# Performance work log

Measured on AMD Instinct MI355X. Metric: run time of the kernel, lower is better.

## Reference

```python
import jax, jax.numpy as jnp
import numpy as np

B = 4; P = 4096; N = B * P          # octree leaf nodes at this depth, equal per sample
ND = N // 8; K = 27                 # stride-2 output nodes; 3x3x3 stencil taps
CIN = 128; COUT = 256; G = 32       # channels, groupnorm groups
H = 16; DH = COUT // H              # attention heads
LCTX = 77; CTX = 768                # context tokens / dim
EPS = 1e-5


def octree_conv(x, neigh, W, b):
    # x: [M_in, Cin], neigh: [M_out, K] (-1 = missing neighbor), W: [K, Cin, Cout]
    mask = (neigh >= 0).astype(x.dtype)[..., None]
    g = x[jnp.maximum(neigh, 0)] * mask            # [M_out, K, Cin]
    return jnp.einsum('nkc,kcd->nd', g, W) + b


def octree_group_norm(x, gamma, beta):
    # per-sample, per-group stats over (nodes-in-sample, channels-in-group)
    n, c = x.shape
    xr = x.reshape(B, n // B, G, c // G)
    mean = xr.mean(axis=(1, 3), keepdims=True)
    var = xr.var(axis=(1, 3), keepdims=True)
    xn = (xr - mean) * jax.lax.rsqrt(var + EPS)
    return xn.reshape(n, c) * gamma + beta


def layer_norm(x, w, b):
    mu = x.mean(-1, keepdims=True)
    var = x.var(-1, keepdims=True)
    return (x - mu) * jax.lax.rsqrt(var + EPS) * w + b


def cross_attention(x, context, ln_w, ln_b, wq, bq, wk, bk, wv, bv, wo, bo):
    # equal points per sample -> per-sample ragged loop == batched attention
    xn = layer_norm(x, ln_w, ln_b).reshape(B, P, COUT)
    q = (xn @ wq + bq).reshape(B, P, H, DH)
    k = (context @ wk + bk).reshape(B, LCTX, H, DH)
    v = (context @ wv + bv).reshape(B, LCTX, H, DH)
    scores = jnp.einsum('bphd,blhd->bhpl', q, k) / np.float32(np.sqrt(DH))
    attn = jax.nn.softmax(scores, axis=-1)
    o = jnp.einsum('bhpl,blhd->bphd', attn, v).reshape(B, P, COUT)
    return x + (o @ wo + bo).reshape(N, COUT)


def reference(x, context, neigh, neigh_down,
              g1_w, g1_b, conv1_w, conv1_b, g2_w, g2_b, conv2_w, conv2_b,
              sc_w, sc_b, ln_w, ln_b, wq, bq, wk, bk, wv, bv, wo, bo,
              down_w, down_b):
    # ResnetBlock
    res = x
    h = jax.nn.silu(octree_group_norm(x, g1_w, g1_b))
    h = octree_conv(h, neigh, conv1_w, conv1_b)
    h = jax.nn.silu(octree_group_norm(h, g2_w, g2_b))
    h = octree_conv(h, neigh, conv2_w, conv2_b)
    h = h + (res @ sc_w + sc_b)                      # Conv1x1 shortcut, skip_scale=1
    # CrossAttention
    h = cross_attention(h, context, ln_w, ln_b, wq, bq, wk, bk, wv, bv, wo, bo)
    # stride-2 downsample conv
    x_down = octree_conv(h, neigh_down, down_w, down_b)
    return (x_down, h)


def setup_inputs():
    key = jax.random.key(0)
    ks = jax.random.split(key, 16)
    w = lambda k, shape, s=0.02: jax.random.normal(k, shape, jnp.float32) * s
    return dict(
        x=w(ks[0], (N, CIN), 1.0),
        context=w(ks[1], (B, LCTX, CTX), 1.0),
        neigh=jax.random.randint(ks[2], (N, K), -3, N, dtype=jnp.int32),
        neigh_down=jax.random.randint(ks[3], (ND, K), -3, N, dtype=jnp.int32),
        g1_w=jnp.ones(CIN), g1_b=jnp.zeros(CIN),
        conv1_w=w(ks[4], (K, CIN, COUT)), conv1_b=jnp.zeros(COUT),
        g2_w=jnp.ones(COUT), g2_b=jnp.zeros(COUT),
        conv2_w=w(ks[5], (K, COUT, COUT)), conv2_b=jnp.zeros(COUT),
        sc_w=w(ks[6], (CIN, COUT)), sc_b=jnp.zeros(COUT),
        ln_w=jnp.ones(COUT), ln_b=jnp.zeros(COUT),
        wq=w(ks[7], (COUT, COUT)), bq=jnp.zeros(COUT),
        wk=w(ks[8], (CTX, COUT)), bk=jnp.zeros(COUT),
        wv=w(ks[9], (CTX, COUT)), bv=jnp.zeros(COUT),
        wo=w(ks[10], (COUT, COUT)), bo=jnp.zeros(COUT),
        down_w=w(ks[11], (K, COUT, COUT)), down_b=jnp.zeros(COUT),
    )
```

## Files before the change

kernel.cpp:

```cpp
#include <hip/hip_runtime.h>
#include <stdint.h>

typedef unsigned short u16;
typedef unsigned int   u32;
typedef __attribute__((ext_vector_type(8))) __bf16 bf16x8;
typedef __attribute__((ext_vector_type(4))) float  f32x4;

__device__ __forceinline__ float bflo(u32 u){ return __uint_as_float(u << 16); }
__device__ __forceinline__ float bfhi(u32 u){ return __uint_as_float(u & 0xffff0000u); }
__device__ __forceinline__ float bf2f(u16 v){ return __uint_as_float(((u32)v) << 16); }
__device__ __forceinline__ u16 f2bf(float f){ u32 u = __float_as_uint(f);
    return (u16)((u + 0x7fffu + ((u >> 16) & 1u)) >> 16); }
__device__ __forceinline__ u32 pack2(float a, float b){ return (u32)f2bf(a) | ((u32)f2bf(b) << 16); }

union ABu { f32x4 f; bf16x8 b; };
__device__ __forceinline__ bf16x8 ldfrag(const u16* p){ ABu u; u.f = *(const f32x4*)p; return u.b; }

__global__ void zero_kernel(u32* p){ p[threadIdx.x] = 0u; }

__global__ __launch_bounds__(256) void bias_init(float* out, const float* b)
{ out[(size_t)blockIdx.x * 256 + threadIdx.x] = b[threadIdx.x]; }

__global__ __launch_bounds__(256)
void transpose_one(const float* __restrict__ in, u16* __restrict__ out, int R)
{
    const int r0 = blockIdx.y * 32, c0 = blockIdx.x * 32;
    __shared__ u16 t[32][33];
    const int tx = threadIdx.x & 31, ty = threadIdx.x >> 5;
    #pragma unroll
    for (int i = 0; i < 4; ++i)
        t[ty + i*8][tx] = f2bf(in[(size_t)(r0 + ty + i*8) * 256 + c0 + tx]);
    __syncthreads();
    #pragma unroll
    for (int i = 0; i < 4; ++i)
        out[(size_t)(c0 + ty + i*8) * R + r0 + tx] = t[tx][ty + i*8];
}

template<int C, int CPG, int IF32>
__global__ __launch_bounds__(256)
void gn_silu_kernel(const void* __restrict__ xv, const float* __restrict__ gw,
                    const float* __restrict__ gb, u16* __restrict__ y)
{
    const int b = blockIdx.x >> 5, g = blockIdx.x & 31;
    const size_t base = (size_t)b * 4096 * C + g * CPG;
    float s = 0.f, ss = 0.f;
    for (int p = threadIdx.x; p < 4096; p += 256) {
        if constexpr (IF32) {
            const float* rp = (const float*)xv + base + (size_t)p * C;
            #pragma unroll
            for (int c = 0; c < CPG; ++c) { const float v = rp[c]; s += v; ss += v*v; }
        } else {
            const u32* rp = (const u32*)((const u16*)xv + base + (size_t)p * C);
            #pragma unroll
            for (int c = 0; c < CPG/2; ++c) {
                const u32 u = rp[c];
                const float v0 = bflo(u), v1 = bfhi(u);
                s += v0 + v1; ss += v0*v0 + v1*v1;
            }
        }
    }
    __shared__ float sbuf[8];
    const int wave = threadIdx.x >> 6, lane = threadIdx.x & 63;
    #pragma unroll
    for (int o = 32; o > 0; o >>= 1) { s += __shfl_down(s, o); ss += __shfl_down(ss, o); }
    if (lane == 0) { sbuf[wave] = s; sbuf[4 + wave] = ss; }
    __syncthreads();
    s  = sbuf[0] + sbuf[1] + sbuf[2] + sbuf[3];
    ss = sbuf[4] + sbuf[5] + sbuf[6] + sbuf[7];
    constexpr float invn = 1.f / (4096.f * CPG);
    const float mean = s * invn;
    const float rstd = rsqrtf(ss * invn - mean * mean + 1e-5f);
    float ga[CPG], be[CPG];
    #pragma unroll
    for (int c = 0; c < CPG; ++c) { ga[c] = gw[g*CPG + c] * rstd; be[c] = gb[g*CPG + c]; }
    for (int p = threadIdx.x; p < 4096; p += 256) {
        u32* wp = (u32*)(y + base + (size_t)p * C);
        float v[CPG];
        if constexpr (IF32) {
            const float* rp = (const float*)xv + base + (size_t)p * C;
            #pragma unroll
            for (int c = 0; c < CPG; ++c) v[c] = rp[c];
        } else {
            const u32* rp = (const u32*)((const u16*)xv + base + (size_t)p * C);
            #pragma unroll
            for (int c = 0; c < CPG/2; ++c) { const u32 u = rp[c]; v[2*c] = bflo(u); v[2*c+1] = bfhi(u); }
        }
        #pragma unroll
        for (int c = 0; c < CPG/2; ++c) {
            float v0 = (v[2*c]   - mean) * ga[2*c]   + be[2*c];
            float v1 = (v[2*c+1] - mean) * ga[2*c+1] + be[2*c+1];
            v0 = v0 / (1.f + __expf(-v0));
            v1 = v1 / (1.f + __expf(-v1));
            wp[c] = pack2(v0, v1);
        }
    }
}

__global__ __launch_bounds__(256)
void ln_kernel(const float* __restrict__ h, const float* __restrict__ w,
               const float* __restrict__ b, u16* __restrict__ y)
{
    const int row = blockIdx.x * 4 + (threadIdx.x >> 6);
    const int lane = threadIdx.x & 63;
    const f32x4 v = *(const f32x4*)(h + (size_t)row * 256 + lane * 4);
    float s  = v[0] + v[1] + v[2] + v[3];
    float ss = v[0]*v[0] + v[1]*v[1] + v[2]*v[2] + v[3]*v[3];
    #pragma unroll
    for (int o = 32; o > 0; o >>= 1) { s += __shfl_down(s, o); ss += __shfl_down(ss, o); }
    s = __shfl(s, 0); ss = __shfl(ss, 0);
    const float mean = s * (1.f/256.f);
    const float rstd = rsqrtf(ss * (1.f/256.f) - mean*mean + 1e-5f);
    const int c = lane * 4;
    const float o0 = (v[0]-mean)*rstd*w[c+0] + b[c+0];
    const float o1 = (v[1]-mean)*rstd*w[c+1] + b[c+1];
    const float o2 = (v[2]-mean)*rstd*w[c+2] + b[c+2];
    const float o3 = (v[3]-mean)*rstd*w[c+3] + b[c+3];
    u32* wp = (u32*)(y + (size_t)row * 256 + c);
    wp[0] = pack2(o0, o1); wp[1] = pack2(o2, o3);
}

__global__ __launch_bounds__(256)
void attn_kernel(const u16* __restrict__ q, const float* __restrict__ kf,
                 const float* __restrict__ vf, u16* __restrict__ o)
{
    const int h = blockIdx.x, b = blockIdx.y, pc = blockIdx.z;
    __shared__ float kS[77*16], vS[77*16];
    for (int i = threadIdx.x; i < 77*16; i += 256) {
        const int l = i >> 4, d = i & 15;
        const size_t src = (size_t)(b*77 + l) * 256 + h*16 + d;
        kS[i] = kf[src];
        vS[i] = vf[src];
    }
    __syncthreads();
    for (int p = pc*512 + threadIdx.x; p < pc*512 + 512; p += 256) {
        const size_t row = (size_t)b * 4096 + p;
        const u32* qp = (const u32*)(q + row * 256 + h * 16);
        float qv[16];
        #pragma unroll
        for (int d2 = 0; d2 < 8; ++d2) { const u32 u = qp[d2]; qv[2*d2] = bflo(u); qv[2*d2+1] = bfhi(u); }
        float m = -1e30f;
        for (int l = 0; l < 77; ++l) {
            float sc = 0.f;
            #pragma unroll
            for (int d = 0; d < 16; ++d) sc += qv[d] * kS[l*16 + d];
            m = fmaxf(m, sc);
        }
        float ssum = 0.f, oacc[16];
        #pragma unroll
        for (int d = 0; d < 16; ++d) oacc[d] = 0.f;
        for (int l = 0; l < 77; ++l) {
            float sc = 0.f;
            #pragma unroll
            for (int d = 0; d < 16; ++d) sc += qv[d] * kS[l*16 + d];
            const float pw = __expf((sc - m) * 0.25f);
            ssum += pw;
            #pragma unroll
            for (int d = 0; d < 16; ++d) oacc[d] += pw * vS[l*16 + d];
        }
        const float inv = 1.f / ssum;
        u32* op = (u32*)(o + row * 256 + h * 16);
        #pragma unroll
        for (int d2 = 0; d2 < 8; ++d2) op[d2] = pack2(oacc[2*d2]*inv, oacc[2*d2+1]*inv);
    }
}

template<int GATHER, int CIN, int RES, int OMODE, int AF32, int SPLITK>
__global__ __launch_bounds__(256, 4)
void gemm_kernel(const void* __restrict__ A, const u16* __restrict__ Bt,
                 const int* __restrict__ neigh, const float* __restrict__ bias,
                 const float* __restrict__ bias2, const float* __restrict__ resid,
                 void* __restrict__ out, u16* __restrict__ out2,
                 const u16* __restrict__ zbuf,
                 const int Mvalid, const int Ktot, const int Nin, const int ksteps)
{
    __shared__ u16 lA[128 * 64];
    __shared__ u16 lB[64 * 64];
    const int tid  = threadIdx.x;
    const int wave = tid >> 6, lane = tid & 63;
    const int quad = lane >> 4, l16 = lane & 15;
    const int mBase = blockIdx.x * 128;
    const int nBase = blockIdx.y * 64;
    const int kbeg = SPLITK ? blockIdx.z * ksteps * 64 : 0;
    const int kend = SPLITK ? kbeg + ksteps * 64 : Ktot;

    int aCofs[4], gm4[4];
    #pragma unroll
    for (int it = 0; it < 4; ++it) {
        const int chunk = (wave * 4 + it) * 64 + lane;
        aCofs[it] = (chunk & 7) * 8;
        gm4[it]   = mBase + (chunk >> 3);
    }
    int bRow[2], bCofs[2];
    #pragma unroll
    for (int it = 0; it < 2; ++it) {
        const int chunk = (wave * 2 + it) * 64 + lane;
        bRow[it]  = nBase + (chunk >> 3);
        bCofs[it] = (chunk & 7) * 8;
    }

    auto issueIdx = [&](int k0, int* dst) {
        if constexpr (GATHER) {
            const int j27 = k0 / CIN;
            #pragma unroll
            for (int it = 0; it < 4; ++it)
                dst[it] = (gm4[it] < Mvalid) ? neigh[gm4[it] * 27 + j27] : -1;
        }
    };
    auto issueA = [&](int k0, const int* idx, f32x4* va) {
        #pragma unroll
        for (int it = 0; it < 4; ++it) {
            if constexpr (GATHER) {
                const int cb = k0 % CIN;
                const u16* src = ((u32)idx[it] < (u32)Nin)
                    ? ((const u16*)A + (size_t)idx[it] * CIN + cb + aCofs[it])
                    : (zbuf + aCofs[it]);
                va[it] = *(const f32x4*)src;
            } else if constexpr (AF32) {
                const float* src = (gm4[it] < Mvalid)
                    ? ((const float*)A + (size_t)gm4[it] * Ktot + k0 + aCofs[it])
                    : ((const float*)zbuf + aCofs[it]);
                const f32x4 lo = ((const f32x4*)src)[0];
                const f32x4 hi = ((const f32x4*)src)[1];
                u32 w4[4] = { pack2(lo[0],lo[1]), pack2(lo[2],lo[3]),
                              pack2(hi[0],hi[1]), pack2(hi[2],hi[3]) };
                va[it] = *(const f32x4*)w4;
            } else {
                const u16* src = (gm4[it] < Mvalid)
                    ? ((const u16*)A + (size_t)gm4[it] * Ktot + k0 + aCofs[it])
                    : (zbuf + aCofs[it]);
                va[it] = *(const f32x4*)src;
            }
        }
    };
    auto issueB = [&](int k0, f32x4* vb) {
        #pragma unroll
        for (int it = 0; it < 2; ++it)
            vb[it] = *(const f32x4*)(Bt + (size_t)bRow[it] * Ktot + k0 + bCofs[it]);
    };
    auto storeLDS = [&](const f32x4* va, const f32x4* vb) {
        #pragma unroll
        for (int it = 0; it < 4; ++it) {
            const int chunk = (wave * 4 + it) * 64 + lane;
            const int row = chunk >> 3, g = chunk & 7;
            *(f32x4*)&lA[row * 64 + ((g ^ (row & 7)) << 3)] = va[it];
        }
        #pragma unroll
        for (int it = 0; it < 2; ++it) {
            const int chunk = (wave * 2 + it) * 64 + lane;
            const int row = chunk >> 3, g = chunk & 7;
            *(f32x4*)&lB[row * 64 + ((g ^ (row & 7)) << 3)] = vb[it];
        }
    };

    f32x4 acc[2][4];
    #pragma unroll
    for (int i = 0; i < 2; ++i)
        #pragma unroll
        for (int j = 0; j < 4; ++j)
            acc[i][j] = (f32x4){0.f, 0.f, 0.f, 0.f};

    auto mfmaPhase = [&]() {
        #pragma unroll
        for (int kk2 = 0; kk2 < 2; ++kk2) {
            const int grp = (((quad + kk2 * 4) ^ (l16 & 7)) << 3);
            bf16x8 bfr[4], af[2];
            #pragma unroll
            for (int j = 0; j < 4; ++j)
                bfr[j] = ldfrag(&lB[(j*16 + l16) * 64 + grp]);
            #pragma unroll
            for (int i = 0; i < 2; ++i)
                af[i] = ldfrag(&lA[(wave*32 + i*16 + l16) * 64 + grp]);
            #pragma unroll
            for (int i = 0; i < 2; ++i)
                #pragma unroll
                for (int j = 0; j < 4; ++j)
                    acc[i][j] = __builtin_amdgcn_mfma_f32_16x16x32_bf16(af[i], bfr[j], acc[i][j], 0, 0, 0);
        }
    };

    int idxP[4], idxQ[4];
    f32x4 va[4], vb[2];
    issueIdx(kbeg, idxP);
    issueA(kbeg, idxP, va);
    issueB(kbeg, vb);
    issueIdx(kbeg + 64 < kend ? kbeg + 64 : kbeg, idxQ);

    for (int k0 = kbeg; k0 < kend; k0 += 128) {
        {
            __syncthreads();
            storeLDS(va, vb);
            __syncthreads();
            const int kn = k0 + 64  < kend ? k0 + 64  : k0;
            const int ki = k0 + 128 < kend ? k0 + 128 : kn;
            issueA(kn, idxQ, va);
            issueB(kn, vb);
            issueIdx(ki, idxP);
            mfmaPhase();
        }
        {
            __syncthreads();
            storeLDS(va, vb);
            __syncthreads();
            const int k1 = k0 + 64;
            const int kn = k1 + 64  < kend ? k1 + 64  : k1;
            const int ki = k1 + 128 < kend ? k1 + 128 : kn;
            issueA(kn, idxP, va);
            issueB(kn, vb);
            issueIdx(ki, idxQ);
            mfmaPhase();
        }
    }

    #pragma unroll
    for (int j = 0; j < 4; ++j) {
        const int col = nBase + j*16 + l16;
        float bv = 0.f;
        if constexpr (!SPLITK) { bv = bias[col]; if (bias2) bv += bias2[col]; }
        #pragma unroll
        for (int i = 0; i < 2; ++i) {
            const int row0 = mBase + wave*32 + i*16 + quad*4;
            #pragma unroll
            for (int r = 0; r < 4; ++r) {
                const int row = row0 + r;
                if (row < Mvalid) {
                    const size_t off = (size_t)row * 256 + col;
                    float v = acc[i][j][r] + bv;
                    if constexpr (SPLITK) {
                        atomicAdd((float*)out + off, v);
                    } else {
                        if constexpr (RES) v += resid[off];
                        if constexpr (OMODE == 0) ((u16*)out)[off] = f2bf(v);
                        else {
                            ((float*)out)[off] = v;
                            if constexpr (OMODE == 2) out2[off] = f2bf(v);
                        }
                    }
                }
            }
        }
    }
}

extern "C" void kernel_launch(void* const* d_in, const int* in_sizes, int n_in,
                              void* d_out, int out_size, void* d_ws, size_t ws_size,
                              hipStream_t stream)
{
    const float* x    = (const float*)d_in[0];
    const float* ctx  = (const float*)d_in[1];
    const int* neigh  = (const int*)d_in[2];
    const int* neighd = (const int*)d_in[3];
    const float* g1w = (const float*)d_in[4];
    const float* g1b = (const float*)d_in[5];
    const float* w1  = (const float*)d_in[6];
    const float* b1  = (const float*)d_in[7];
    const float* g2w = (const float*)d_in[8];
    const float* g2b = (const float*)d_in[9];
    const float* w2  = (const float*)d_in[10];
    const float* b2  = (const float*)d_in[11];
    const float* scw = (const float*)d_in[12];
    const float* scb = (const float*)d_in[13];
    const float* lnw = (const float*)d_in[14];
    const float* lnb = (const float*)d_in[15];
    const float* wq  = (const float*)d_in[16];
    const float* bq  = (const float*)d_in[17];
    const float* wk  = (const float*)d_in[18];
    const float* bk  = (const float*)d_in[19];
    const float* wv  = (const float*)d_in[20];
    const float* bv  = (const float*)d_in[21];
    const float* wo  = (const float*)d_in[22];
    const float* bo  = (const float*)d_in[23];
    const float* dw  = (const float*)d_in[24];
    const float* db  = (const float*)d_in[25];

    float* out0 = (float*)d_out;
    float* H5   = (float*)d_out + (size_t)2048 * 256;
    float* KF   = (float*)d_out;
    float* VF   = KF + (size_t)308 * 256;

    char* p = (char*)d_ws;
    auto alloc = [&](size_t bytes) { char* r = p; p += (bytes + 255) & ~(size_t)255; return r; };
    u16* zbuf = (u16*)alloc(512);
    u16* S0   = (u16*)alloc((size_t)16384*256*2);
    u16* S3   = (u16*)alloc((size_t)16384*256*2);
    u16* WtB  = (u16*)alloc((size_t)27*256*256*2);
    u16* scT  = (u16*)alloc((size_t)128*256*2);
    u16* wqT  = (u16*)alloc((size_t)256*256*2);
    u16* wkT  = (u16*)alloc((size_t)768*256*2);
    u16* wvT  = (u16*)alloc((size_t)768*256*2);
    u16* woT  = (u16*)alloc((size_t)256*256*2);

    zero_kernel<<<1, 128, 0, stream>>>((u32*)zbuf);
    transpose_one<<<dim3(8,4),   256, 0, stream>>>(scw, scT, 128);
    transpose_one<<<dim3(8,8),   256, 0, stream>>>(wq,  wqT, 256);
    transpose_one<<<dim3(8,24),  256, 0, stream>>>(wk,  wkT, 768);
    transpose_one<<<dim3(8,24),  256, 0, stream>>>(wv,  wvT, 768);
    transpose_one<<<dim3(8,8),   256, 0, stream>>>(wo,  woT, 256);
    transpose_one<<<dim3(8,108), 256, 0, stream>>>(w1,  WtB, 3456);

    gn_silu_kernel<128,4,1><<<128, 256, 0, stream>>>(x, g1w, g1b, S0);
    bias_init<<<16384, 256, 0, stream>>>(H5, b1);
    gemm_kernel<1,128,0,1,0,1><<<dim3(128,4,3), 256, 0, stream>>>(S0, WtB, neigh, nullptr, nullptr, nullptr, H5, nullptr, zbuf, 16384, 3456, 16384, 18);
    gn_silu_kernel<256,8,1><<<128, 256, 0, stream>>>(H5, g2w, g2b, S0);
    gemm_kernel<0,1,0,1,1,0><<<dim3(128,4), 256, 0, stream>>>(x, scT, nullptr, scb, b2, nullptr, H5, nullptr, zbuf, 16384, 128, 0, 0);
    transpose_one<<<dim3(8,216), 256, 0, stream>>>(w2, WtB, 6912);
    gemm_kernel<1,256,0,1,0,1><<<dim3(128,4,3), 256, 0, stream>>>(S0, WtB, neigh, nullptr, nullptr, nullptr, H5, nullptr, zbuf, 16384, 6912, 16384, 36);
    ln_kernel<<<4096, 256, 0, stream>>>(H5, lnw, lnb, S0);
    gemm_kernel<0,1,0,0,0,0><<<dim3(128,4), 256, 0, stream>>>(S0, wqT, nullptr, bq, nullptr, nullptr, S3, nullptr, zbuf, 16384, 256, 0, 0);
    gemm_kernel<0,1,0,1,1,0><<<dim3(3,4),   256, 0, stream>>>(ctx, wkT, nullptr, bk, nullptr, nullptr, KF, nullptr, zbuf, 308, 768, 0, 0);
    gemm_kernel<0,1,0,1,1,0><<<dim3(3,4),   256, 0, stream>>>(ctx, wvT, nullptr, bv, nullptr, nullptr, VF, nullptr, zbuf, 308, 768, 0, 0);
    attn_kernel<<<dim3(16,4,8), 256, 0, stream>>>(S3, KF, VF, S0);
    gemm_kernel<0,1,1,2,0,0><<<dim3(128,4), 256, 0, stream>>>(S0, woT, nullptr, bo, nullptr, H5, H5, S3, zbuf, 16384, 256, 0, 0);
    transpose_one<<<dim3(8,216), 256, 0, stream>>>(dw, WtB, 6912);
    bias_init<<<2048, 256, 0, stream>>>(out0, db);
    gemm_kernel<1,256,0,1,0,1><<<dim3(16,4,6), 256, 0, stream>>>(S3, WtB, neighd, nullptr, nullptr, nullptr, out0, nullptr, zbuf, 2048, 6912, 16384, 18);
}
```

Baseline: 547.1 us.

## Widen GEMM tile to 128x128 and batch all weight transposes into one launch

Grows the GEMM block tile from 128x64 to 128x128, with 2x2 waves each computing a 64x64 subtile. This doubles the MFMA work per LDS load and halves re-gathering of the A rows across N tiles, at the cost of more registers and LDS (occupancy hint lowered to 2). All weight transposes and the zero-buffer init are merged into one 3D-grid launch writing separate buffers, removing several small launches. The downsample conv split-K is raised to 18 to keep the grid filled.

```diff
diff --git a/kernel.cpp b/kernel.cpp
--- a/kernel.cpp
+++ b/kernel.cpp
@@ -16,15 +16,22 @@
 union ABu { f32x4 f; bf16x8 b; };
 __device__ __forceinline__ bf16x8 ldfrag(const u16* p){ ABu u; u.f = *(const f32x4*)p; return u.b; }
 
-__global__ void zero_kernel(u32* p){ p[threadIdx.x] = 0u; }
-
 __global__ __launch_bounds__(256) void bias_init(float* out, const float* b)
 { out[(size_t)blockIdx.x * 256 + threadIdx.x] = b[threadIdx.x]; }
 
+struct TArgs { const float* in[8]; u16* out[8]; int R[8]; };
 __global__ __launch_bounds__(256)
-void transpose_one(const float* __restrict__ in, u16* __restrict__ out, int R)
-{
-    const int r0 = blockIdx.y * 32, c0 = blockIdx.x * 32;
+void transpose_all(TArgs a, u32* zbuf)
+{
+    if (blockIdx.x == 0 && blockIdx.y == 0 && blockIdx.z == 0 && threadIdx.x < 128)
+        zbuf[threadIdx.x] = 0u;
+    const int mid = blockIdx.z;
+    const int R = a.R[mid];
+    const int r0 = blockIdx.y * 32;
+    if (r0 >= R) return;
+    const int c0 = blockIdx.x * 32;
+    const float* __restrict__ in = a.in[mid];
+    u16* __restrict__ out = a.out[mid];
     __shared__ u16 t[32][33];
     const int tx = threadIdx.x & 31, ty = threadIdx.x >> 5;
     #pragma unroll
@@ -165,7 +172,7 @@
 }
 
 template<int GATHER, int CIN, int RES, int OMODE, int AF32, int SPLITK>
-__global__ __launch_bounds__(256, 4)
+__global__ __launch_bounds__(256, 2)
 void gemm_kernel(const void* __restrict__ A, const u16* __restrict__ Bt,
                  const int* __restrict__ neigh, const float* __restrict__ bias,
                  const float* __restrict__ bias2, const float* __restrict__ resid,
@@ -174,28 +181,24 @@
                  const int Mvalid, const int Ktot, const int Nin, const int ksteps)
 {
     __shared__ u16 lA[128 * 64];
-    __shared__ u16 lB[64 * 64];
+    __shared__ u16 lB[128 * 64];
     const int tid  = threadIdx.x;
     const int wave = tid >> 6, lane = tid & 63;
+    const int wr = wave >> 1, wc = wave & 1;
     const int quad = lane >> 4, l16 = lane & 15;
     const int mBase = blockIdx.x * 128;
-    const int nBase = blockIdx.y * 64;
+    const int nBase = blockIdx.y * 128;
     const int kbeg = SPLITK ? blockIdx.z * ksteps * 64 : 0;
     const int kend = SPLITK ? kbeg + ksteps * 64 : Ktot;
 
-    int aCofs[4], gm4[4];
+    int aCofs[4], gm4[4], bRow[4], bCofs[4];
     #pragma unroll
     for (int it = 0; it < 4; ++it) {
         const int chunk = (wave * 4 + it) * 64 + lane;
         aCofs[it] = (chunk & 7) * 8;
         gm4[it]   = mBase + (chunk >> 3);
-    }
-    int bRow[2], bCofs[2];
-    #pragma unroll
-    for (int it = 0; it < 2; ++it) {
-        const int chunk = (wave * 2 + it) * 64 + lane;
         bRow[it]  = nBase + (chunk >> 3);
-        bCofs[it] = (chunk & 7) * 8;
+        bCofs[it] = aCofs[it];
     }
 
     auto issueIdx = [&](int k0, int* dst) {
@@ -234,7 +237,7 @@
     };
     auto issueB = [&](int k0, f32x4* vb) {
         #pragma unroll
-        for (int it = 0; it < 2; ++it)
+        for (int it = 0; it < 4; ++it)
             vb[it] = *(const f32x4*)(Bt + (size_t)bRow[it] * Ktot + k0 + bCofs[it]);
     };
     auto storeLDS = [&](const f32x4* va, const f32x4* vb) {
@@ -243,18 +246,13 @@
             const int chunk = (wave * 4 + it) * 64 + lane;
             const int row = chunk >> 3, g = chunk & 7;
             *(f32x4*)&lA[row * 64 + ((g ^ (row & 7)) << 3)] = va[it];
-        }
-        #pragma unroll
-        for (int it = 0; it < 2; ++it) {
-            const int chunk = (wave * 2 + it) * 64 + lane;
-            const int row = chunk >> 3, g = chunk & 7;
             *(f32x4*)&lB[row * 64 + ((g ^ (row & 7)) << 3)] = vb[it];
         }
     };
 
-    f32x4 acc[2][4];
-    #pragma unroll
-    for (int i = 0; i < 2; ++i)
+    f32x4 acc[4][4];
+    #pragma unroll
+    for (int i = 0; i < 4; ++i)
         #pragma unroll
         for (int j = 0; j < 4; ++j)
             acc[i][j] = (f32x4){0.f, 0.f, 0.f, 0.f};
@@ -263,15 +261,15 @@
         #pragma unroll
         for (int kk2 = 0; kk2 < 2; ++kk2) {
             const int grp = (((quad + kk2 * 4) ^ (l16 & 7)) << 3);
-            bf16x8 bfr[4], af[2];
+            bf16x8 bfr[4], af[4];
             #pragma unroll
             for (int j = 0; j < 4; ++j)
-                bfr[j] = ldfrag(&lB[(j*16 + l16) * 64 + grp]);
-            #pragma unroll
-            for (int i = 0; i < 2; ++i)
-                af[i] = ldfrag(&lA[(wave*32 + i*16 + l16) * 64 + grp]);
-            #pragma unroll
-            for (int i = 0; i < 2; ++i)
+                bfr[j] = ldfrag(&lB[(wc*64 + j*16 + l16) * 64 + grp]);
+            #pragma unroll
+            for (int i = 0; i < 4; ++i)
+                af[i] = ldfrag(&lA[(wr*64 + i*16 + l16) * 64 + grp]);
+            #pragma unroll
+            for (int i = 0; i < 4; ++i)
                 #pragma unroll
                 for (int j = 0; j < 4; ++j)
                     acc[i][j] = __builtin_amdgcn_mfma_f32_16x16x32_bf16(af[i], bfr[j], acc[i][j], 0, 0, 0);
@@ -279,7 +277,7 @@
     };
 
     int idxP[4], idxQ[4];
-    f32x4 va[4], vb[2];
+    f32x4 va[4], vb[4];
     issueIdx(kbeg, idxP);
     issueA(kbeg, idxP, va);
     issueB(kbeg, vb);
@@ -313,12 +311,12 @@
 
     #pragma unroll
     for (int j = 0; j < 4; ++j) {
-        const int col = nBase + j*16 + l16;
+        const int col = nBase + wc*64 + j*16 + l16;
         float bv = 0.f;
         if constexpr (!SPLITK) { bv = bias[col]; if (bias2) bv += bias2[col]; }
         #pragma unroll
-        for (int i = 0; i < 2; ++i) {
-            const int row0 = mBase + wave*32 + i*16 + quad*4;
+        for (int i = 0; i < 4; ++i) {
+            const int row0 = mBase + wr*64 + i*16 + quad*4;
             #pragma unroll
             for (int r = 0; r < 4; ++r) {
                 const int row = row0 + r;
@@ -382,35 +380,38 @@
     u16* zbuf = (u16*)alloc(512);
     u16* S0   = (u16*)alloc((size_t)16384*256*2);
     u16* S3   = (u16*)alloc((size_t)16384*256*2);
-    u16* WtB  = (u16*)alloc((size_t)27*256*256*2);
+    u16* Wt1  = (u16*)alloc((size_t)27*128*256*2);
+    u16* Wt2  = (u16*)alloc((size_t)27*256*256*2);
+    u16* WtD  = (u16*)alloc((size_t)27*256*256*2);
     u16* scT  = (u16*)alloc((size_t)128*256*2);
     u16* wqT  = (u16*)alloc((size_t)256*256*2);
     u16* wkT  = (u16*)alloc((size_t)768*256*2);
     u16* wvT  = (u16*)alloc((size_t)768*256*2);
     u16* woT  = (u16*)alloc((size_t)256*256*2);
 
-    zero_kernel<<<1, 128, 0, stream>>>((u32*)zbuf);
-    transpose_one<<<dim3(8,4),   256, 0, stream>>>(scw, scT, 128);
-    transpose_one<<<dim3(8,8),   256, 0, stream>>>(wq,  wqT, 256);
-    transpose_one<<<dim3(8,24),  256, 0, stream>>>(wk,  wkT, 768);
-    transpose_one<<<dim3(8,24),  256, 0, stream>>>(wv,  wvT, 768);
-    transpose_one<<<dim3(8,8),   256, 0, stream>>>(wo,  woT, 256);
-    transpose_one<<<dim3(8,108), 256, 0, stream>>>(w1,  WtB, 3456);
+    TArgs ta;
+    ta.in[0]=w1;  ta.out[0]=Wt1; ta.R[0]=3456;
+    ta.in[1]=w2;  ta.out[1]=Wt2; ta.R[1]=6912;
+    ta.in[2]=dw;  ta.out[2]=WtD; ta.R[2]=6912;
+    ta.in[3]=scw; ta.out[3]=scT; ta.R[3]=128;
+    ta.in[4]=wq;  ta.out[4]=wqT; ta.R[4]=256;
+    ta.in[5]=wk;  ta.out[5]=wkT; ta.R[5]=768;
+    ta.in[6]=wv;  ta.out[6]=wvT; ta.R[6]=768;
+    ta.in[7]=wo;  ta.out[7]=woT; ta.R[7]=256;
+    transpose_all<<<dim3(8, 216, 8), 256, 0, stream>>>(ta, (u32*)zbuf);
 
     gn_silu_kernel<128,4,1><<<128, 256, 0, stream>>>(x, g1w, g1b, S0);
     bias_init<<<16384, 256, 0, stream>>>(H5, b1);
-    gemm_kernel<1,128,0,1,0,1><<<dim3(128,4,3), 256, 0, stream>>>(S0, WtB, neigh, nullptr, nullptr, nullptr, H5, nullptr, zbuf, 16384, 3456, 16384, 18);
+    gemm_kernel<1,128,0,1,0,1><<<dim3(128,2,3), 256, 0, stream>>>(S0, Wt1, neigh, nullptr, nullptr, nullptr, H5, nullptr, zbuf, 16384, 3456, 16384, 18);
     gn_silu_kernel<256,8,1><<<128, 256, 0, stream>>>(H5, g2w, g2b, S0);
-    gemm_kernel<0,1,0,1,1,0><<<dim3(128,4), 256, 0, stream>>>(x, scT, nullptr, scb, b2, nullptr, H5, nullptr, zbuf, 16384, 128, 0, 0);
-    transpose_one<<<dim3(8,216), 256, 0, stream>>>(w2, WtB, 6912);
-    gemm_kernel<1,256,0,1,0,1><<<dim3(128,4,3), 256, 0, stream>>>(S0, WtB, neigh, nullptr, nullptr, nullptr, H5, nullptr, zbuf, 16384, 6912, 16384, 36);
+    gemm_kernel<0,1,0,1,1,0><<<dim3(128,2), 256, 0, stream>>>(x, scT, nullptr, scb, b2, nullptr, H5, nullptr, zbuf, 16384, 128, 0, 0);
+    gemm_kernel<1,256,0,1,0,1><<<dim3(128,2,3), 256, 0, stream>>>(S0, Wt2, neigh, nullptr, nullptr, nullptr, H5, nullptr, zbuf, 16384, 6912, 16384, 36);
     ln_kernel<<<4096, 256, 0, stream>>>(H5, lnw, lnb, S0);
-    gemm_kernel<0,1,0,0,0,0><<<dim3(128,4), 256, 0, stream>>>(S0, wqT, nullptr, bq, nullptr, nullptr, S3, nullptr, zbuf, 16384, 256, 0, 0);
-    gemm_kernel<0,1,0,1,1,0><<<dim3(3,4),   256, 0, stream>>>(ctx, wkT, nullptr, bk, nullptr, nullptr, KF, nullptr, zbuf, 308, 768, 0, 0);
-    gemm_kernel<0,1,0,1,1,0><<<dim3(3,4),   256, 0, stream>>>(ctx, wvT, nullptr, bv, nullptr, nullptr, VF, nullptr, zbuf, 308, 768, 0, 0);
+    gemm_kernel<0,1,0,0,0,0><<<dim3(128,2), 256, 0, stream>>>(S0, wqT, nullptr, bq, nullptr, nullptr, S3, nullptr, zbuf, 16384, 256, 0, 0);
+    gemm_kernel<0,1,0,1,1,0><<<dim3(3,2),   256, 0, stream>>>(ctx, wkT, nullptr, bk, nullptr, nullptr, KF, nullptr, zbuf, 308, 768, 0, 0);
+    gemm_kernel<0,1,0,1,1,0><<<dim3(3,2),   256, 0, stream>>>(ctx, wvT, nullptr, bv, nullptr, nullptr, VF, nullptr, zbuf, 308, 768, 0, 0);
     attn_kernel<<<dim3(16,4,8), 256, 0, stream>>>(S3, KF, VF, S0);
-    gemm_kernel<0,1,1,2,0,0><<<dim3(128,4), 256, 0, stream>>>(S0, woT, nullptr, bo, nullptr, H5, H5, S3, zbuf, 16384, 256, 0, 0);
-    transpose_one<<<dim3(8,216), 256, 0, stream>>>(dw, WtB, 6912);
+    gemm_kernel<0,1,1,2,0,0><<<dim3(128,2), 256, 0, stream>>>(S0, woT, nullptr, bo, nullptr, H5, H5, S3, zbuf, 16384, 256, 0, 0);
     bias_init<<<2048, 256, 0, stream>>>(out0, db);
-    gemm_kernel<1,256,0,1,0,1><<<dim3(16,4,6), 256, 0, stream>>>(S3, WtB, neighd, nullptr, nullptr, nullptr, out0, nullptr, zbuf, 2048, 6912, 16384, 18);
-}
+    gemm_kernel<1,256,0,1,0,1><<<dim3(16,2,18), 256, 0, stream>>>(S3, WtD, neighd, nullptr, nullptr, nullptr, out0, nullptr, zbuf, 2048, 6912, 16384, 6);
+}
```

New measurement: 602.6 us. 1.1x slower.

## Deepen GEMM prefetch to two stages and batch all weight transposes

Applied to the files above, without the earlier changes.

The GEMM main loop now keeps two register-staged tiles in flight. Global loads for the tile two steps ahead are issued before the MFMA phase, and LDS is written after it, so load latency overlaps compute better. All weight transposes and the zero-buffer init are merged into one launch with separate output buffers, removing several small launches and the serialized re-transposes between GEMMs. The cost is more registers per thread, which may reduce occupancy under launch_bounds(256,4), plus extra workspace memory.

```diff
diff --git a/kernel.cpp b/kernel.cpp
--- a/kernel.cpp
+++ b/kernel.cpp
@@ -16,15 +16,22 @@
 union ABu { f32x4 f; bf16x8 b; };
 __device__ __forceinline__ bf16x8 ldfrag(const u16* p){ ABu u; u.f = *(const f32x4*)p; return u.b; }
 
-__global__ void zero_kernel(u32* p){ p[threadIdx.x] = 0u; }
-
 __global__ __launch_bounds__(256) void bias_init(float* out, const float* b)
 { out[(size_t)blockIdx.x * 256 + threadIdx.x] = b[threadIdx.x]; }
 
+struct TArgs { const float* in[8]; u16* out[8]; int R[8]; };
 __global__ __launch_bounds__(256)
-void transpose_one(const float* __restrict__ in, u16* __restrict__ out, int R)
-{
-    const int r0 = blockIdx.y * 32, c0 = blockIdx.x * 32;
+void transpose_all(TArgs a, u32* zbuf)
+{
+    if (blockIdx.x == 0 && blockIdx.y == 0 && blockIdx.z == 0 && threadIdx.x < 128)
+        zbuf[threadIdx.x] = 0u;
+    const int mid = blockIdx.z;
+    const int R = a.R[mid];
+    const int r0 = blockIdx.y * 32;
+    if (r0 >= R) return;
+    const int c0 = blockIdx.x * 32;
+    const float* __restrict__ in = a.in[mid];
+    u16* __restrict__ out = a.out[mid];
     __shared__ u16 t[32][33];
     const int tx = threadIdx.x & 31, ty = threadIdx.x >> 5;
     #pragma unroll
@@ -182,6 +189,7 @@
     const int nBase = blockIdx.y * 64;
     const int kbeg = SPLITK ? blockIdx.z * ksteps * 64 : 0;
     const int kend = SPLITK ? kbeg + ksteps * 64 : Ktot;
+    const int klast = kend - 64;
 
     int aCofs[4], gm4[4];
     #pragma unroll
@@ -278,36 +286,36 @@
         }
     };
 
-    int idxP[4], idxQ[4];
-    f32x4 va[4], vb[2];
-    issueIdx(kbeg, idxP);
-    issueA(kbeg, idxP, va);
-    issueB(kbeg, vb);
-    issueIdx(kbeg + 64 < kend ? kbeg + 64 : kbeg, idxQ);
+    int idxP[4], idxQ[4], i0[4], i1[4];
+    f32x4 aP[4], bP[2], aQ[4], bQ[2];
+    auto kc = [&](int k){ return k <= klast ? k : klast; };
+    issueIdx(kbeg, i0);
+    issueA(kbeg, i0, aP);          issueB(kbeg, bP);
+    issueIdx(kc(kbeg + 64), i1);
+    issueA(kc(kbeg + 64), i1, aQ); issueB(kc(kbeg + 64), bQ);
+    issueIdx(kc(kbeg + 128), idxP);
+    issueIdx(kc(kbeg + 192), idxQ);
+    storeLDS(aP, bP);
+    __syncthreads();
 
     for (int k0 = kbeg; k0 < kend; k0 += 128) {
         {
+            issueA(kc(k0 + 128), idxP, aP);
+            issueB(kc(k0 + 128), bP);
+            issueIdx(kc(k0 + 256), idxP);
+            mfmaPhase();
             __syncthreads();
-            storeLDS(va, vb);
+            storeLDS(aQ, bQ);
             __syncthreads();
-            const int kn = k0 + 64  < kend ? k0 + 64  : k0;
-            const int ki = k0 + 128 < kend ? k0 + 128 : kn;
-            issueA(kn, idxQ, va);
-            issueB(kn, vb);
-            issueIdx(ki, idxP);
+        }
+        {
+            issueA(kc(k0 + 192), idxQ, aQ);
+            issueB(kc(k0 + 192), bQ);
+            issueIdx(kc(k0 + 320), idxQ);
             mfmaPhase();
-        }
-        {
             __syncthreads();
-            storeLDS(va, vb);
+            storeLDS(aP, bP);
             __syncthreads();
-            const int k1 = k0 + 64;
-            const int kn = k1 + 64  < kend ? k1 + 64  : k1;
-            const int ki = k1 + 128 < kend ? k1 + 128 : kn;
-            issueA(kn, idxP, va);
-            issueB(kn, vb);
-            issueIdx(ki, idxQ);
-            mfmaPhase();
         }
     }
 
@@ -382,35 +390,38 @@
     u16* zbuf = (u16*)alloc(512);
     u16* S0   = (u16*)alloc((size_t)16384*256*2);
     u16* S3   = (u16*)alloc((size_t)16384*256*2);
-    u16* WtB  = (u16*)alloc((size_t)27*256*256*2);
+    u16* Wt1  = (u16*)alloc((size_t)27*128*256*2);
+    u16* Wt2  = (u16*)alloc((size_t)27*256*256*2);
+    u16* WtD  = (u16*)alloc((size_t)27*256*256*2);
     u16* scT  = (u16*)alloc((size_t)128*256*2);
     u16* wqT  = (u16*)alloc((size_t)256*256*2);
     u16* wkT  = (u16*)alloc((size_t)768*256*2);
     u16* wvT  = (u16*)alloc((size_t)768*256*2);
     u16* woT  = (u16*)alloc((size_t)256*256*2);
 
-    zero_kernel<<<1, 128, 0, stream>>>((u32*)zbuf);
-    transpose_one<<<dim3(8,4),   256, 0, stream>>>(scw, scT, 128);
-    transpose_one<<<dim3(8,8),   256, 0, stream>>>(wq,  wqT, 256);
-    transpose_one<<<dim3(8,24),  256, 0, stream>>>(wk,  wkT, 768);
-    transpose_one<<<dim3(8,24),  256, 0, stream>>>(wv,  wvT, 768);
-    transpose_one<<<dim3(8,8),   256, 0, stream>>>(wo,  woT, 256);
-    transpose_one<<<dim3(8,108), 256, 0, stream>>>(w1,  WtB, 3456);
+    TArgs ta;
+    ta.in[0]=w1;  ta.out[0]=Wt1; ta.R[0]=3456;
+    ta.in[1]=w2;  ta.out[1]=Wt2; ta.R[1]=6912;
+    ta.in[2]=dw;  ta.out[2]=WtD; ta.R[2]=6912;
+    ta.in[3]=scw; ta.out[3]=scT; ta.R[3]=128;
+    ta.in[4]=wq;  ta.out[4]=wqT; ta.R[4]=256;
+    ta.in[5]=wk;  ta.out[5]=wkT; ta.R[5]=768;
+    ta.in[6]=wv;  ta.out[6]=wvT; ta.R[6]=768;
+    ta.in[7]=wo;  ta.out[7]=woT; ta.R[7]=256;
+    transpose_all<<<dim3(8, 216, 8), 256, 0, stream>>>(ta, (u32*)zbuf);
 
     gn_silu_kernel<128,4,1><<<128, 256, 0, stream>>>(x, g1w, g1b, S0);
     bias_init<<<16384, 256, 0, stream>>>(H5, b1);
-    gemm_kernel<1,128,0,1,0,1><<<dim3(128,4,3), 256, 0, stream>>>(S0, WtB, neigh, nullptr, nullptr, nullptr, H5, nullptr, zbuf, 16384, 3456, 16384, 18);
+    gemm_kernel<1,128,0,1,0,1><<<dim3(128,4,3), 256, 0, stream>>>(S0, Wt1, neigh, nullptr, nullptr, nullptr, H5, nullptr, zbuf, 16384, 3456, 16384, 18);
     gn_silu_kernel<256,8,1><<<128, 256, 0, stream>>>(H5, g2w, g2b, S0);
     gemm_kernel<0,1,0,1,1,0><<<dim3(128,4), 256, 0, stream>>>(x, scT, nullptr, scb, b2, nullptr, H5, nullptr, zbuf, 16384, 128, 0, 0);
-    transpose_one<<<dim3(8,216), 256, 0, stream>>>(w2, WtB, 6912);
-    gemm_kernel<1,256,0,1,0,1><<<dim3(128,4,3), 256, 0, stream>>>(S0, WtB, neigh, nullptr, nullptr, nullptr, H5, nullptr, zbuf, 16384, 6912, 16384, 36);
+    gemm_kernel<1,256,0,1,0,1><<<dim3(128,4,3), 256, 0, stream>>>(S0, Wt2, neigh, nullptr, nullptr, nullptr, H5, nullptr, zbuf, 16384, 6912, 16384, 36);
     ln_kernel<<<4096, 256, 0, stream>>>(H5, lnw, lnb, S0);
     gemm_kernel<0,1,0,0,0,0><<<dim3(128,4), 256, 0, stream>>>(S0, wqT, nullptr, bq, nullptr, nullptr, S3, nullptr, zbuf, 16384, 256, 0, 0);
     gemm_kernel<0,1,0,1,1,0><<<dim3(3,4),   256, 0, stream>>>(ctx, wkT, nullptr, bk, nullptr, nullptr, KF, nullptr, zbuf, 308, 768, 0, 0);
     gemm_kernel<0,1,0,1,1,0><<<dim3(3,4),   256, 0, stream>>>(ctx, wvT, nullptr, bv, nullptr, nullptr, VF, nullptr, zbuf, 308, 768, 0, 0);
     attn_kernel<<<dim3(16,4,8), 256, 0, stream>>>(S3, KF, VF, S0);
     gemm_kernel<0,1,1,2,0,0><<<dim3(128,4), 256, 0, stream>>>(S0, woT, nullptr, bo, nullptr, H5, H5, S3, zbuf, 16384, 256, 0, 0);
-    transpose_one<<<dim3(8,216), 256, 0, stream>>>(dw, WtB, 6912);
     bias_init<<<2048, 256, 0, stream>>>(out0, db);
-    gemm_kernel<1,256,0,1,0,1><<<dim3(16,4,6), 256, 0, stream>>>(S3, WtB, neighd, nullptr, nullptr, nullptr, out0, nullptr, zbuf, 2048, 6912, 16384, 18);
-}
+    gemm_kernel<1,256,0,1,0,1><<<dim3(16,4,6), 256, 0, stream>>>(S3, WtD, neighd, nullptr, nullptr, nullptr, out0, nullptr, zbuf, 2048, 6912, 16384, 18);
+}
```

After: 692.1 us. 1.27x slower.
